# Kernel optimization log

Measured on AMD Instinct MI355X. Metric: run time of the kernel, lower is better.

The kernel has to match this reference:

```python
import jax, jax.numpy as jnp
import numpy as np

EPS = 1e-5

def _bn(x, g, b):
    # BatchNorm1d in training mode: biased batch variance, eps=1e-5
    mu = jnp.mean(x, axis=0)
    var = jnp.var(x, axis=0)
    return g * (x - mu) * jax.lax.rsqrt(var + EPS) + b

def _prelu(x, a):
    return jnp.where(x >= 0, x, a * x)

def setup_inputs() -> dict:
    key = jax.random.key(0)
    ks = jax.random.split(key, 32)
    B, MF, E = 4096, 128, 64
    f32 = jnp.float32

    def lin_w(k, o, i):
        bound = 1.0 / np.sqrt(i)
        return jax.random.uniform(k, (o, i), f32, -bound, bound)

    def lin_b(k, o, i):
        bound = 1.0 / np.sqrt(i)
        return jax.random.uniform(k, (o,), f32, -bound, bound)

    def exp_w(k, e, o, i):
        bound = 1.0 / np.sqrt(i)
        return jax.random.uniform(k, (e, o, i), f32, -bound, bound)

    def exp_b(k, e, o, i):
        bound = 1.0 / np.sqrt(i)
        return jax.random.uniform(k, (e, o), f32, -bound, bound)

    quarter = jnp.full((1,), 0.25, f32)  # PReLU default init
    return {
        'm0': jax.random.normal(ks[0], (B, MF), f32),
        'x0': jax.random.normal(ks[1], (B, 64), f32),
        'mW1': lin_w(ks[2], 256, 128), 'mb1': lin_b(ks[3], 256, 128),
        'mg1': jnp.ones((256,), f32), 'mbe1': jnp.zeros((256,), f32), 'ma1': quarter,
        'mW2': lin_w(ks[4], 128, 256), 'mb2': lin_b(ks[5], 128, 256),
        'mg2': jnp.ones((128,), f32), 'mbe2': jnp.zeros((128,), f32), 'ma2': quarter,
        'mW3': lin_w(ks[6], 64, 128), 'mb3': lin_b(ks[7], 64, 128),
        'mg3': jnp.ones((64,), f32), 'mbe3': jnp.zeros((64,), f32), 'ma3': quarter,
        'Wenc0': exp_w(ks[8], E, 256, 64), 'benc0': exp_b(ks[9], E, 256, 64),
        'Wenc1': exp_w(ks[10], E, 256, 256), 'benc1': exp_b(ks[11], E, 256, 256),
        'Wdec0': exp_w(ks[12], E, 256, 256), 'bdec0': exp_b(ks[13], E, 256, 256),
        'Wdec1': exp_w(ks[14], E, 64, 256), 'bdec1': exp_b(ks[15], E, 64, 256),
        'bng': jnp.ones((256,), f32), 'bnb': jnp.zeros((256,), f32), 'a': quarter,
    }

def reference(m0, x0, mW1, mb1, mg1, mbe1, ma1, mW2, mb2, mg2, mbe2, ma2,
              mW3, mb3, mg3, mbe3, ma3, Wenc0, benc0, Wenc1, benc1,
              Wdec0, bdec0, Wdec1, bdec1, bng, bnb, a):
    # m_encoder (MNet): Linear+BN+PReLU x3 -> per-sample expert weights [B, 64]
    h = _prelu(_bn(m0 @ mW1.T + mb1, mg1, mbe1), ma1)
    h = _prelu(_bn(h @ mW2.T + mb2, mg2, mbe2), ma2)
    w = _prelu(_bn(h @ mW3.T + mb3, mg3, mbe3), ma3)  # [B, E]

    w_sum = jnp.sum(w)           # scalar sum over all B*E, as in torch code
    wn = w / w_sum               # [B, E]

    def experts(z, W, b):
        # all-experts dense combine: sum_e wn[b,e] * (z @ W_e^T + b_e)
        h = jnp.einsum('bi,eoi->beo', z, W) + b  # [B, E, O]
        return jnp.einsum('beo,be->bo', h, wn)

    # encoder: depth=2, BN+PReLU after each layer (shared bn(256) and PReLU)
    z = _prelu(_bn(experts(x0, Wenc0, benc0), bng, bnb), a)
    z = _prelu(_bn(experts(z, Wenc1, benc1), bng, bnb), a)
    # decoder: BN+PReLU on all but last layer
    y = _prelu(_bn(experts(z, Wdec0, bdec0), bng, bnb), a)
    y = experts(y, Wdec1, bdec1)  # [B, 64]
    return y
```

## Files before the change

### kernel.cpp

```cpp
#include <hip/hip_runtime.h>
#include <stdint.h>

#define BATCH 4096
#define NEXP 64

typedef __bf16 bf16x8 __attribute__((ext_vector_type(8)));
typedef float f32x4 __attribute__((ext_vector_type(4)));
typedef float f32x8 __attribute__((ext_vector_type(8)));
typedef unsigned int u32x4 __attribute__((ext_vector_type(4)));
typedef unsigned short u16x4 __attribute__((ext_vector_type(4)));
typedef unsigned short u16x8 __attribute__((ext_vector_type(8)));

__device__ __forceinline__ unsigned short f2bf(float f) {
  unsigned u = __builtin_bit_cast(unsigned, f);
  u += 0x7fffu + ((u >> 16) & 1u);
  return (unsigned short)(u >> 16);
}

__device__ __forceinline__ void async_copy16(const void* g, void* l) {
  __builtin_amdgcn_global_load_lds(
      (const __attribute__((address_space(1))) void*)(uintptr_t)g,
      (__attribute__((address_space(3))) void*)(uintptr_t)l, 16, 0, 0);
}

enum { AM_PLAIN = 0, AM_BN = 1 };

template <int BM_, int BN_, int WR, int WC, int AMODE>
__global__ __launch_bounds__(256, 4) void gemm_k(
    const float* __restrict__ Af32, const float* __restrict__ scv,
    const float* __restrict__ shv, const float* __restrict__ alphaPtr,
    const unsigned short* __restrict__ PB, int K, int nsubsTot,
    float* __restrict__ Cp, const float* __restrict__ biasv, int N,
    int ktilesTot) {
  constexpr int MS = BM_ / 16;
  constexpr int NS = BN_ / 16;
  constexpr int WTM = BM_ / WR, WTN = BN_ / WC;
  constexpr int TM = WTM / 16, TN = WTN / 16;
  constexpr int PCH = MS / 2;

  __shared__ __align__(16) unsigned short As[2 * MS * 512];
  __shared__ __align__(16) unsigned short Bs[2 * NS * 512];

  const int tid = threadIdx.x;
  const int lane = tid & 63;
  const int wid = tid >> 6;
  const int wrow = wid / WC, wcol = wid % WC;

  const int m0 = blockIdx.x * BM_;
  const int ntile = blockIdx.y;
  const int n0 = ntile * BN_;

  float alpha = 0.f;
  if constexpr (AMODE == AM_BN) alpha = alphaPtr[0];

  f32x4 acc[TM][TN] = {};

  for (int kt = 0; kt < ktilesTot; ++kt) {
    const int k0 = kt * 64;

    for (int f = wid; f < 2 * NS; f += 4) {
      const int fkt = f / NS, fns = f % NS;
      const long fragIdx = (long)(k0 / 32 + fkt) * nsubsTot + (ntile * NS + fns);
      async_copy16(PB + fragIdx * 512 + lane * 8, &Bs[f * 512 + lane * 8]);
    }

#pragma unroll
    for (int p = 0; p < PCH; ++p) {
      const int id = p * 256 + tid;
      const int fA = id >> 6;
      const int q = id & 63;
      const int ksh = fA / MS, msub = fA % MS;
      const int kq = q >> 4, mrow = q & 15;
      const int m = msub * 16 + mrow;
      const int kg = k0 + ksh * 32 + kq * 8;
      const long mg = m0 + m;
      f32x8 vf;
      if constexpr (AMODE == AM_PLAIN) {
        const f32x4* src = (const f32x4*)(Af32 + mg * K + kg);
        f32x4 a0 = src[0], a1 = src[1];
#pragma unroll
        for (int j = 0; j < 4; ++j) { vf[j] = a0[j]; vf[4 + j] = a1[j]; }
      } else {
        const f32x4* src = (const f32x4*)(Af32 + mg * K + kg);
        f32x4 a0 = src[0], a1 = src[1];
        f32x4 s0 = *(const f32x4*)(scv + kg), s1 = *(const f32x4*)(scv + kg + 4);
        f32x4 h0 = *(const f32x4*)(shv + kg), h1 = *(const f32x4*)(shv + kg + 4);
#pragma unroll
        for (int j = 0; j < 4; ++j) {
          float v = fmaf(a0[j], s0[j], h0[j]);
          vf[j] = v >= 0.f ? v : alpha * v;
          float v2 = fmaf(a1[j], s1[j], h1[j]);
          vf[4 + j] = v2 >= 0.f ? v2 : alpha * v2;
        }
      }
      bf16x8 ob = __builtin_convertvector(vf, bf16x8);
      *(u16x8*)&As[id * 8] = __builtin_bit_cast(u16x8, ob);
    }
    __syncthreads();

#pragma unroll
    for (int ks = 0; ks < 2; ++ks) {
      bf16x8 af[TM], bfr[TN];
#pragma unroll
      for (int i = 0; i < TM; ++i) {
        const int msub = wrow * TM + i;
        af[i] = __builtin_bit_cast(
            bf16x8, *(const u32x4*)&As[(ks * MS + msub) * 512 + lane * 8]);
      }
#pragma unroll
      for (int j = 0; j < TN; ++j) {
        const int nsub = wcol * TN + j;
        bfr[j] = __builtin_bit_cast(
            bf16x8, *(const u32x4*)&Bs[(ks * NS + nsub) * 512 + lane * 8]);
      }
#pragma unroll
      for (int i = 0; i < TM; ++i)
#pragma unroll
        for (int j = 0; j < TN; ++j)
          acc[i][j] = __builtin_amdgcn_mfma_f32_16x16x32_bf16(af[i], bfr[j],
                                                              acc[i][j], 0, 0, 0);
    }
    __syncthreads();
  }

  const int q = lane >> 4, nn = lane & 15;
#pragma unroll
  for (int i = 0; i < TM; ++i) {
    const int rowb = m0 + wrow * WTM + i * 16 + q * 4;
#pragma unroll
    for (int j = 0; j < TN; ++j) {
      const int col = n0 + wcol * WTN + j * 16 + nn;
      const float bv = biasv ? biasv[col] : 0.f;
#pragma unroll
      for (int r = 0; r < 4; ++r)
        Cp[(long)(rowb + r) * N + col] = acc[i][j][r] + bv;
    }
  }
}

template <int BN_, int KE_, int EPB, int NTILE>
__global__ __launch_bounds__(256, 2) void egemm_k(
    const unsigned short* __restrict__ zpk, const float* __restrict__ wnT,
    const float* __restrict__ bias, const unsigned short* __restrict__ PB,
    float* __restrict__ Cbase, long partStride, int N, int nsubsTot) {
  constexpr int KT2 = KE_ / 32;
  constexpr int NS = BN_ / 16;
  constexpr int TN = NS / 4;
  constexpr int TM = 4;
  constexpr int NC = NTILE * (NEXP / EPB);
  constexpr int T = EPB * KT2;
  constexpr int U = ((KT2 & 3) == 0) ? 1 : (4 / KT2);

  const int tid = threadIdx.x, lane = tid & 63, wid = tid >> 6;
  const int bx = blockIdx.x;
  const int combo = bx % NC;
  const int mb = bx / NC;
  const int ntile = combo % NTILE;
  const int slice = combo / NTILE;
  const int e0 = slice * EPB;
  const int n0 = ntile * BN_;
  float* __restrict__ Cp = Cbase + (long)slice * partStride;
  const int nn = lane & 15, q = lane >> 4;

  float bvAll[EPB * TN];
#pragma unroll
  for (int ei = 0; ei < EPB; ++ei)
#pragma unroll
    for (int j = 0; j < TN; ++j)
      bvAll[ei * TN + j] =
          bias[(long)(e0 + ei) * N + n0 + wid * (TN * 16) + j * 16 + nn];

  const unsigned short* Aw = zpk + (long)mb * (KT2 * 4 * 512);
  u32x4 areg[TM][KT2];
#pragma unroll
  for (int i = 0; i < TM; ++i)
#pragma unroll
    for (int kt = 0; kt < KT2; ++kt)
      areg[i][kt] = *(const u32x4*)(Aw + (kt * 4 + i) * 512 + lane * 8);

  const long kstr = (long)nsubsTot * 512;
  const unsigned short* Bt = PB + (long)e0 * KT2 * kstr +
                             ((long)ntile * NS + wid * TN) * 512 + lane * 8;

  u32x4 ring[4][TN];
#pragma unroll
  for (int t = 0; t < 4; ++t)
#pragma unroll
    for (int j = 0; j < TN; ++j)
      ring[t][j] = *(const u32x4*)(Bt + (long)t * kstr + j * 512);

  f32x4 mainAcc[TM][TN] = {};

  for (int eb = 0; eb < EPB; eb += U) {
#pragma unroll
    for (int u = 0; u < U; ++u) {
      const int ei = eb + u;
      const int e = e0 + ei;
      f32x4 tmp[TM][TN];
#pragma unroll
      for (int j = 0; j < TN; ++j) {
        const float bv = bvAll[ei * TN + j];
        f32x4 t4 = {bv, bv, bv, bv};
#pragma unroll
        for (int i = 0; i < TM; ++i) tmp[i][j] = t4;
      }
#pragma unroll
      for (int kt = 0; kt < KT2; ++kt) {
        const int slot = (u * KT2 + kt) & 3;
#pragma unroll
        for (int i = 0; i < TM; ++i) {
          bf16x8 af = __builtin_bit_cast(bf16x8, areg[i][kt]);
#pragma unroll
          for (int j = 0; j < TN; ++j)
            tmp[i][j] = __builtin_amdgcn_mfma_f32_16x16x32_bf16(
                af, __builtin_bit_cast(bf16x8, ring[slot][j]), tmp[i][j], 0, 0,
                0);
        }
        {
          const int t = ei * KT2 + kt;
          const int tl = (t + 4 < T) ? (t + 4) : (T - 1);
#pragma unroll
          for (int j = 0; j < TN; ++j)
            ring[slot][j] = *(const u32x4*)(Bt + (long)tl * kstr + j * 512);
        }
      }
#pragma unroll
      for (int i = 0; i < TM; ++i) {
        const int rowb = mb * 64 + i * 16 + q * 4;
        f32x4 wn4 = *(const f32x4*)(wnT + (long)e * BATCH + rowb);
#pragma unroll
        for (int j = 0; j < TN; ++j) mainAcc[i][j] += wn4 * tmp[i][j];
      }
    }
  }

#pragma unroll
  for (int i = 0; i < TM; ++i) {
    const int rowb = mb * 64 + i * 16 + q * 4;
#pragma unroll
    for (int j = 0; j < TN; ++j) {
      const int col = n0 + wid * (TN * 16) + j * 16 + nn;
#pragma unroll
      for (int r = 0; r < 4; ++r)
        Cp[(long)(rowb + r) * N + col] = mainAcc[i][j][r];
    }
  }
}

__global__ void hstats_k(float* __restrict__ P, long partStride, int nparts,
                         int C, float* __restrict__ S1, float* __restrict__ S2) {
  const int c0 = blockIdx.x * 4;
  const int r0 = blockIdx.y * (BATCH / 8);
  f32x4 s = {0.f, 0.f, 0.f, 0.f}, s2 = {0.f, 0.f, 0.f, 0.f};
  for (int r = r0 + threadIdx.x; r < r0 + BATCH / 8; r += 256) {
    f32x4 x = *(const f32x4*)(P + (long)r * C + c0);
    for (int p = 1; p < nparts; ++p)
      x += *(const f32x4*)(P + p * partStride + (long)r * C + c0);
    *(f32x4*)(P + (long)r * C + c0) = x;
    s += x;
    s2 += x * x;
  }
  __shared__ f32x4 sb[256], qb[256];
  sb[threadIdx.x] = s;
  qb[threadIdx.x] = s2;
  __syncthreads();
  for (int st = 128; st > 0; st >>= 1) {
    if (threadIdx.x < st) {
      sb[threadIdx.x] += sb[threadIdx.x + st];
      qb[threadIdx.x] += qb[threadIdx.x + st];
    }
    __syncthreads();
  }
  if (threadIdx.x < 4) {
    atomicAdd(&S1[c0 + threadIdx.x], sb[0][threadIdx.x]);
    atomicAdd(&S2[c0 + threadIdx.x], qb[0][threadIdx.x]);
  }
}

__global__ void stats_k(const float* __restrict__ H, int C,
                        const float* __restrict__ g, const float* __restrict__ b,
                        float* __restrict__ scv, float* __restrict__ shv) {
  const int c0 = blockIdx.x * 4;
  f32x4 s = {0.f, 0.f, 0.f, 0.f}, s2 = {0.f, 0.f, 0.f, 0.f};
  for (int r = threadIdx.x; r < BATCH; r += 256) {
    f32x4 x = *(const f32x4*)(H + (long)r * C + c0);
    s += x;
    s2 += x * x;
  }
  __shared__ f32x4 sb[256], qb[256];
  sb[threadIdx.x] = s;
  qb[threadIdx.x] = s2;
  __syncthreads();
  for (int st = 128; st > 0; st >>= 1) {
    if (threadIdx.x < st) {
      sb[threadIdx.x] += sb[threadIdx.x + st];
      qb[threadIdx.x] += qb[threadIdx.x + st];
    }
    __syncthreads();
  }
  if (threadIdx.x < 4) {
    const int c = c0 + threadIdx.x;
    float mu = sb[0][threadIdx.x] * (1.f / BATCH);
    float var = qb[0][threadIdx.x] * (1.f / BATCH) - mu * mu;
    float isig = 1.f / sqrtf(var + 1e-5f);
    float sc_ = g[c] * isig;
    scv[c] = sc_;
    shv[c] = b[c] - mu * sc_;
  }
}

__global__ void zbuild_pk(const float* __restrict__ H,
                          const float* __restrict__ S1,
                          const float* __restrict__ S2,
                          const float* __restrict__ g,
                          const float* __restrict__ b,
                          const float* __restrict__ alphaPtr,
                          unsigned short* __restrict__ zpk) {
  const int c = blockIdx.x * 256 + threadIdx.x;
  const float alpha = alphaPtr[0];
  const int mb = c >> 11, r = c & 2047;
  const int kt = r >> 8, q2 = r & 255;
  const int msub = q2 >> 6, ln = q2 & 63;
  const int row = mb * 64 + msub * 16 + (ln & 15);
  const int col = kt * 32 + (ln >> 4) * 8;
  const float* src = H + (long)row * 256 + col;
  u16x8 o;
#pragma unroll
  for (int h = 0; h < 2; ++h) {
    f32x4 a = *(const f32x4*)(src + h * 4);
    f32x4 s1 = *(const f32x4*)(S1 + col + h * 4);
    f32x4 s2 = *(const f32x4*)(S2 + col + h * 4);
    f32x4 gv = *(const f32x4*)(g + col + h * 4);
    f32x4 bv = *(const f32x4*)(b + col + h * 4);
#pragma unroll
    for (int j = 0; j < 4; ++j) {
      float mu = s1[j] * (1.f / BATCH);
      float var = s2[j] * (1.f / BATCH) - mu * mu;
      float sc_ = gv[j] / sqrtf(var + 1e-5f);
      float sh_ = bv[j] - mu * sc_;
      float v = fmaf(a[j], sc_, sh_);
      v = v >= 0.f ? v : alpha * v;
      o[h * 4 + j] = f2bf(v);
    }
  }
  *(u16x8*)(zpk + (long)c * 8) = o;
}

__global__ void wbuild_k(const float* __restrict__ G, const float* __restrict__ scv,
                         const float* __restrict__ shv,
                         const float* __restrict__ alphaPtr,
                         float* __restrict__ w, float* __restrict__ wsum) {
  const int idx = blockIdx.x * 256 + threadIdx.x;
  const float alpha = alphaPtr[0];
  const int c0 = (idx * 4) & 63;
  f32x4 x = *(const f32x4*)(G + (long)idx * 4);
  f32x4 sv = *(const f32x4*)(scv + c0);
  f32x4 hv = *(const f32x4*)(shv + c0);
  f32x4 o;
  float part = 0.f;
#pragma unroll
  for (int j = 0; j < 4; ++j) {
    float v = fmaf(x[j], sv[j], hv[j]);
    v = v >= 0.f ? v : alpha * v;
    o[j] = v;
    part += v;
  }
  *(f32x4*)(w + (long)idx * 4) = o;
  __shared__ float sb[256];
  sb[threadIdx.x] = part;
  __syncthreads();
  for (int st = 128; st > 0; st >>= 1) {
    if (threadIdx.x < st) sb[threadIdx.x] += sb[threadIdx.x + st];
    __syncthreads();
  }
  if (threadIdx.x == 0) atomicAdd(wsum, sb[0]);
}

__global__ void wnTcast_k(const float* __restrict__ w,
                          const float* __restrict__ wsum,
                          float* __restrict__ wnT, const float* __restrict__ x0,
                          unsigned short* __restrict__ x0pk) {
  const int bx = blockIdx.x;
  if (bx < 1024) {
    const int idx = bx * 256 + threadIdx.x;
    const int e = idx >> 12, b = idx & 4095;
    wnT[idx] = w[(long)b * NEXP + e] * (1.0f / wsum[0]);
  } else {
    const int c = (bx - 1024) * 256 + threadIdx.x;
    const int mb = c >> 9, r = c & 511;
    const int kt = r >> 8, q2 = r & 255;
    const int msub = q2 >> 6, ln = q2 & 63;
    const int row = mb * 64 + msub * 16 + (ln & 15);
    const int col = kt * 32 + (ln >> 4) * 8;
    const float* src = x0 + (long)row * 64 + col;
    f32x4 a0 = *(const f32x4*)src, a1 = *(const f32x4*)(src + 4);
    u16x8 o;
#pragma unroll
    for (int j = 0; j < 4; ++j) {
      o[j] = f2bf(a0[j]);
      o[4 + j] = f2bf(a1[j]);
    }
    *(u16x8*)(x0pk + (long)c * 8) = o;
  }
}

__global__ void prepackall_k(
    const float* __restrict__ w0, const float* __restrict__ w1,
    const float* __restrict__ w2, const float* __restrict__ w3,
    const float* __restrict__ w4, const float* __restrict__ w5,
    const float* __restrict__ w6, unsigned short* __restrict__ PB) {
  const int t = blockIdx.x * 256 + threadIdx.x;
  const float* W;
  int nsubs, shI;
  long loc;
  if (t < 4096) { W = w0; nsubs = 16; shI = 7; loc = t; }
  else if (t < 8192) { W = w1; nsubs = 8; shI = 8; loc = t - 4096; }
  else if (t < 9216) { W = w2; nsubs = 4; shI = 7; loc = t - 8192; }
  else if (t < 140288) { W = w3; nsubs = 16; shI = 6; loc = t - 9216; }
  else if (t < 664576) { W = w4; nsubs = 16; shI = 8; loc = t - 140288; }
  else if (t < 1188864) { W = w5; nsubs = 16; shI = 8; loc = t - 664576; }
  else if (t < 1319936) { W = w6; nsubs = 4; shI = 8; loc = t - 1188864; }
  else return;
  const int lane = (int)(loc & 63);
  const long frag = loc >> 6;
  const int nsub = (int)(frag % nsubs);
  const long ktile = frag / nsubs;
  const int n = nsub * 16 + (lane & 15);
  const int k = (int)(ktile * 32 + (lane >> 4) * 8);
  const int e = k >> shI;
  const int i0 = k & ((1 << shI) - 1);
  const int O = nsubs * 16;
  const float* src = W + ((long)e * O + n) * (1 << shI) + i0;
  f32x4 a0 = *(const f32x4*)src, a1 = *(const f32x4*)(src + 4);
  u16x8 o;
#pragma unroll
  for (int j = 0; j < 4; ++j) {
    o[j] = f2bf(a0[j]);
    o[4 + j] = f2bf(a1[j]);
  }
  *(u16x8*)(PB + (long)t * 8) = o;
}

__global__ void reduceN_k(const float* __restrict__ P, long partStride, int nparts,
                          float* __restrict__ out, int total4) {
  const int idx = blockIdx.x * 256 + threadIdx.x;
  if (idx >= total4) return;
  f32x4 s = {0.f, 0.f, 0.f, 0.f};
  for (int p = 0; p < nparts; ++p)
    s += *(const f32x4*)(P + p * partStride + (long)idx * 4);
  *(f32x4*)(out + (long)idx * 4) = s;
}

extern "C" void kernel_launch(void* const* d_in, const int* in_sizes, int n_in,
                              void* d_out, int out_size, void* d_ws, size_t ws_size,
                              hipStream_t stream) {
  const float* m0 = (const float*)d_in[0];
  const float* x0 = (const float*)d_in[1];
  const float* mW1 = (const float*)d_in[2];
  const float* mb1 = (const float*)d_in[3];
  const float* mg1 = (const float*)d_in[4];
  const float* mbe1 = (const float*)d_in[5];
  const float* ma1 = (const float*)d_in[6];
  const float* mW2 = (const float*)d_in[7];
  const float* mb2 = (const float*)d_in[8];
  const float* mg2 = (const float*)d_in[9];
  const float* mbe2 = (const float*)d_in[10];
  const float* ma2 = (const float*)d_in[11];
  const float* mW3 = (const float*)d_in[12];
  const float* mb3 = (const float*)d_in[13];
  const float* mg3 = (const float*)d_in[14];
  const float* mbe3 = (const float*)d_in[15];
  const float* ma3 = (const float*)d_in[16];
  const float* Wenc0 = (const float*)d_in[17];
  const float* benc0 = (const float*)d_in[18];
  const float* Wenc1 = (const float*)d_in[19];
  const float* benc1 = (const float*)d_in[20];
  const float* Wdec0 = (const float*)d_in[21];
  const float* bdec0 = (const float*)d_in[22];
  const float* Wdec1 = (const float*)d_in[23];
  const float* bdec1 = (const float*)d_in[24];
  const float* bng = (const float*)d_in[25];
  const float* bnb = (const float*)d_in[26];
  const float* aexp = (const float*)d_in[27];

  const int SPL = 4;
  const int SPLD = 8;

  char* base = (char*)d_ws;
  size_t off = 0;
  auto alloc = [&](size_t bytes) {
    void* p = base + off;
    off = (off + bytes + 255) & ~(size_t)255;
    return p;
  };
  unsigned short* PB = (unsigned short*)alloc(1319936L * 16);
  const long CO_mW2 = 4096, CO_mW3 = 8192, CO_e0 = 9216, CO_e1 = 140288,
             CO_d0 = 664576, CO_d1 = 1188864;
  float* Pb = (float*)alloc((size_t)SPL * BATCH * 256 * 4);
  float* P0 = Pb;
  float* P1 = Pb + (long)BATCH * 256;
  unsigned short* zApk = (unsigned short*)alloc(BATCH * 256 * 2);
  unsigned short* zBpk = (unsigned short*)alloc(BATCH * 256 * 2);
  unsigned short* x0pk = (unsigned short*)alloc(BATCH * 64 * 2);
  float* wbuf = (float*)alloc(BATCH * 64 * 4);
  float* wnT = (float*)alloc((size_t)NEXP * BATCH * 4);
  float* scv = (float*)alloc(256 * 4);
  float* shv = (float*)alloc(256 * 4);
  float* zeroBuf = (float*)alloc(8192);
  float* wsum = zeroBuf;
  float* S1a = zeroBuf + 256, *S2a = zeroBuf + 512;
  float* S1b = zeroBuf + 768, *S2b = zeroBuf + 1024;
  float* S1c = zeroBuf + 1280, *S2c = zeroBuf + 1536;

  const dim3 blk(256);
  const long PS = BATCH * 256;

  hipMemsetAsync(zeroBuf, 0, 8192, stream);
  prepackall_k<<<5156, blk, 0, stream>>>(mW1, mW2, mW3, Wenc0, Wenc1, Wdec0,
                                         Wdec1, PB);

  gemm_k<64, 128, 2, 2, AM_PLAIN><<<dim3(64, 2, 1), blk, 0, stream>>>(
      m0, nullptr, nullptr, nullptr, PB, 128, 16, P0, mb1, 256, 2);
  stats_k<<<64, blk, 0, stream>>>(P0, 256, mg1, mbe1, scv, shv);
  gemm_k<64, 128, 2, 2, AM_BN><<<dim3(64, 1, 1), blk, 0, stream>>>(
      P0, scv, shv, ma1, PB + CO_mW2 * 8, 256, 8, P1, mb2, 128, 4);
  stats_k<<<32, blk, 0, stream>>>(P1, 128, mg2, mbe2, scv, shv);
  gemm_k<64, 64, 2, 2, AM_BN><<<dim3(64, 1, 1), blk, 0, stream>>>(
      P1, scv, shv, ma2, PB + CO_mW3 * 8, 128, 4, P0, mb3, 64, 2);
  stats_k<<<16, blk, 0, stream>>>(P0, 64, mg3, mbe3, scv, shv);
  wbuild_k<<<256, blk, 0, stream>>>(P0, scv, shv, ma3, wbuf, wsum);
  wnTcast_k<<<1152, blk, 0, stream>>>(wbuf, wsum, wnT, x0, x0pk);

  egemm_k<128, 64, 16, 2><<<dim3(512), blk, 0, stream>>>(
      x0pk, wnT, benc0, PB + CO_e0 * 8, Pb, PS, 256, 16);
  hstats_k<<<dim3(64, 8), blk, 0, stream>>>(Pb, PS, SPL, 256, S1a, S2a);
  zbuild_pk<<<512, blk, 0, stream>>>(Pb, S1a, S2a, bng, bnb, aexp, zApk);

  egemm_k<128, 256, 16, 2><<<dim3(512), blk, 0, stream>>>(
      zApk, wnT, benc1, PB + CO_e1 * 8, Pb, PS, 256, 16);
  hstats_k<<<dim3(64, 8), blk, 0, stream>>>(Pb, PS, SPL, 256, S1b, S2b);
  zbuild_pk<<<512, blk, 0, stream>>>(Pb, S1b, S2b, bng, bnb, aexp, zBpk);

  egemm_k<128, 256, 16, 2><<<dim3(512), blk, 0, stream>>>(
      zBpk, wnT, bdec0, PB + CO_d0 * 8, Pb, PS, 256, 16);
  hstats_k<<<dim3(64, 8), blk, 0, stream>>>(Pb, PS, SPL, 256, S1c, S2c);
  zbuild_pk<<<512, blk, 0, stream>>>(Pb, S1c, S2c, bng, bnb, aexp, zApk);

  egemm_k<64, 256, 8, 1><<<dim3(512), blk, 0, stream>>>(
      zApk, wnT, bdec1, PB + CO_d1 * 8, Pb, (long)BATCH * 64, 64, 4);
  reduceN_k<<<256, blk, 0, stream>>>(Pb, (long)BATCH * 64, SPLD, (float*)d_out,
                                     65536);

  (void)in_sizes; (void)n_in; (void)out_size; (void)ws_size;
}
```

Measured before the change: 410.8 us.

## Split expert GEMMs along K into halves and restructure partial-sum stats reduction

Adds a KHALVES template parameter to the expert GEMM so each block handles half of the K dimension, writing to separate partial buffers. This doubles the grid size, and halves the register-held A fragments, to improve occupancy and parallelism. It also rewrites hstats_k to use row-group blocks with full-width column coverage and fewer reduction barriers, and chooses the partition count from the workspace size. The cost is more partial-sum traffic, since the reduction kernels must read 8 or 16 partial buffers instead of 4 or 8.

```diff
diff --git a/kernel.cpp b/kernel.cpp
--- a/kernel.cpp
+++ b/kernel.cpp
@@ -138,16 +138,19 @@
   }
 }
 
-template <int BN_, int KE_, int EPB, int NTILE>
+template <int BN_, int KE_, int EPB, int NTILE, int KHALVES>
 __global__ __launch_bounds__(256, 2) void egemm_k(
     const unsigned short* __restrict__ zpk, const float* __restrict__ wnT,
     const float* __restrict__ bias, const unsigned short* __restrict__ PB,
     float* __restrict__ Cbase, long partStride, int N, int nsubsTot) {
-  constexpr int KT2 = KE_ / 32;
+  constexpr int KT2F = KE_ / 32;
+  constexpr int KT2 = KT2F / KHALVES;
+  constexpr int LK = (KT2 == 8) ? 3 : (KT2 == 4) ? 2 : 1;
   constexpr int NS = BN_ / 16;
   constexpr int TN = NS / 4;
   constexpr int TM = 4;
-  constexpr int NC = NTILE * (NEXP / EPB);
+  constexpr int S = NEXP / EPB;
+  constexpr int NC = NTILE * S * KHALVES;
   constexpr int T = EPB * KT2;
   constexpr int U = ((KT2 & 3) == 0) ? 1 : (4 / KT2);
 
@@ -156,57 +159,60 @@
   const int combo = bx % NC;
   const int mb = bx / NC;
   const int ntile = combo % NTILE;
-  const int slice = combo / NTILE;
+  const int rest = combo / NTILE;
+  const int slice = rest % S;
+  const int khalf = rest / S;
   const int e0 = slice * EPB;
   const int n0 = ntile * BN_;
-  float* __restrict__ Cp = Cbase + (long)slice * partStride;
+  float* __restrict__ Cp = Cbase + (long)(khalf * S + slice) * partStride;
   const int nn = lane & 15, q = lane >> 4;
-
-  float bvAll[EPB * TN];
-#pragma unroll
-  for (int ei = 0; ei < EPB; ++ei)
-#pragma unroll
-    for (int j = 0; j < TN; ++j)
-      bvAll[ei * TN + j] =
-          bias[(long)(e0 + ei) * N + n0 + wid * (TN * 16) + j * 16 + nn];
-
-  const unsigned short* Aw = zpk + (long)mb * (KT2 * 4 * 512);
+  const bool addBias = (KHALVES == 1) || (khalf == 0);
+
+  const unsigned short* zb =
+      zpk + (long)mb * (KT2F * 4 * 512) + (long)khalf * (KT2 * 4 * 512);
   u32x4 areg[TM][KT2];
 #pragma unroll
   for (int i = 0; i < TM; ++i)
 #pragma unroll
     for (int kt = 0; kt < KT2; ++kt)
-      areg[i][kt] = *(const u32x4*)(Aw + (kt * 4 + i) * 512 + lane * 8);
+      areg[i][kt] = *(const u32x4*)(zb + (kt * 4 + i) * 512 + lane * 8);
 
   const long kstr = (long)nsubsTot * 512;
-  const unsigned short* Bt = PB + (long)e0 * KT2 * kstr +
+  const unsigned short* Bq = PB + ((long)e0 * KT2F + khalf * KT2) * kstr +
                              ((long)ntile * NS + wid * TN) * 512 + lane * 8;
+  auto baddr = [&](int u) {
+    const int ei = u >> LK, kt = u & (KT2 - 1);
+    return Bq + ((long)ei * KT2F + kt) * kstr;
+  };
 
   u32x4 ring[4][TN];
 #pragma unroll
-  for (int t = 0; t < 4; ++t)
-#pragma unroll
-    for (int j = 0; j < TN; ++j)
-      ring[t][j] = *(const u32x4*)(Bt + (long)t * kstr + j * 512);
+  for (int t = 0; t < 4; ++t) {
+    const unsigned short* a = baddr(t < T ? t : T - 1);
+#pragma unroll
+    for (int j = 0; j < TN; ++j) ring[t][j] = *(const u32x4*)(a + j * 512);
+  }
 
   f32x4 mainAcc[TM][TN] = {};
 
   for (int eb = 0; eb < EPB; eb += U) {
 #pragma unroll
-    for (int u = 0; u < U; ++u) {
-      const int ei = eb + u;
+    for (int uu = 0; uu < U; ++uu) {
+      const int ei = eb + uu;
       const int e = e0 + ei;
       f32x4 tmp[TM][TN];
 #pragma unroll
       for (int j = 0; j < TN; ++j) {
-        const float bv = bvAll[ei * TN + j];
+        const float bv =
+            addBias ? bias[(long)e * N + n0 + wid * (TN * 16) + j * 16 + nn]
+                    : 0.f;
         f32x4 t4 = {bv, bv, bv, bv};
 #pragma unroll
         for (int i = 0; i < TM; ++i) tmp[i][j] = t4;
       }
 #pragma unroll
       for (int kt = 0; kt < KT2; ++kt) {
-        const int slot = (u * KT2 + kt) & 3;
+        const int slot = (uu * KT2 + kt) & 3;
 #pragma unroll
         for (int i = 0; i < TM; ++i) {
           bf16x8 af = __builtin_bit_cast(bf16x8, areg[i][kt]);
@@ -217,11 +223,12 @@
                 0);
         }
         {
-          const int t = ei * KT2 + kt;
-          const int tl = (t + 4 < T) ? (t + 4) : (T - 1);
+          const int u = ei * KT2 + kt;
+          const int un = (u + 4 < T) ? (u + 4) : (T - 1);
+          const unsigned short* a = baddr(un);
 #pragma unroll
           for (int j = 0; j < TN; ++j)
-            ring[slot][j] = *(const u32x4*)(Bt + (long)tl * kstr + j * 512);
+            ring[slot][j] = *(const u32x4*)(a + j * 512);
         }
       }
 #pragma unroll
@@ -248,15 +255,18 @@
 }
 
 __global__ void hstats_k(float* __restrict__ P, long partStride, int nparts,
-                         int C, float* __restrict__ S1, float* __restrict__ S2) {
-  const int c0 = blockIdx.x * 4;
-  const int r0 = blockIdx.y * (BATCH / 8);
+                         float* __restrict__ S1, float* __restrict__ S2) {
+  const int c0 = (threadIdx.x & 63) * 4;
+  const int rg = threadIdx.x >> 6;
+  const int rb = blockIdx.x * 8;
   f32x4 s = {0.f, 0.f, 0.f, 0.f}, s2 = {0.f, 0.f, 0.f, 0.f};
-  for (int r = r0 + threadIdx.x; r < r0 + BATCH / 8; r += 256) {
-    f32x4 x = *(const f32x4*)(P + (long)r * C + c0);
+#pragma unroll
+  for (int it = 0; it < 2; ++it) {
+    const long r = rb + it * 4 + rg;
+    f32x4 x = *(const f32x4*)(P + r * 256 + c0);
     for (int p = 1; p < nparts; ++p)
-      x += *(const f32x4*)(P + p * partStride + (long)r * C + c0);
-    *(f32x4*)(P + (long)r * C + c0) = x;
+      x += *(const f32x4*)(P + p * partStride + r * 256 + c0);
+    *(f32x4*)(P + r * 256 + c0) = x;
     s += x;
     s2 += x * x;
   }
@@ -264,16 +274,17 @@
   sb[threadIdx.x] = s;
   qb[threadIdx.x] = s2;
   __syncthreads();
-  for (int st = 128; st > 0; st >>= 1) {
-    if (threadIdx.x < st) {
-      sb[threadIdx.x] += sb[threadIdx.x + st];
-      qb[threadIdx.x] += qb[threadIdx.x + st];
-    }
-    __syncthreads();
-  }
-  if (threadIdx.x < 4) {
-    atomicAdd(&S1[c0 + threadIdx.x], sb[0][threadIdx.x]);
-    atomicAdd(&S2[c0 + threadIdx.x], qb[0][threadIdx.x]);
+  if (threadIdx.x < 64) {
+    f32x4 ts = sb[threadIdx.x] + sb[64 + threadIdx.x] + sb[128 + threadIdx.x] +
+               sb[192 + threadIdx.x];
+    f32x4 tq = qb[threadIdx.x] + qb[64 + threadIdx.x] + qb[128 + threadIdx.x] +
+               qb[192 + threadIdx.x];
+    const int c = threadIdx.x * 4;
+#pragma unroll
+    for (int j = 0; j < 4; ++j) {
+      atomicAdd(&S1[c + j], ts[j]);
+      atomicAdd(&S2[c + j], tq[j]);
+    }
   }
 }
 
@@ -483,8 +494,8 @@
   const float* bnb = (const float*)d_in[26];
   const float* aexp = (const float*)d_in[27];
 
-  const int SPL = 4;
-  const int SPLD = 8;
+  const bool big = ws_size >= (size_t)62 * 1024 * 1024;
+  const int NPARTS = big ? 8 : 4;
 
   char* base = (char*)d_ws;
   size_t off = 0;
@@ -496,7 +507,7 @@
   unsigned short* PB = (unsigned short*)alloc(1319936L * 16);
   const long CO_mW2 = 4096, CO_mW3 = 8192, CO_e0 = 9216, CO_e1 = 140288,
              CO_d0 = 664576, CO_d1 = 1188864;
-  float* Pb = (float*)alloc((size_t)SPL * BATCH * 256 * 4);
+  float* Pb = (float*)alloc((size_t)NPARTS * BATCH * 256 * 4);
   float* P0 = Pb;
   float* P1 = Pb + (long)BATCH * 256;
   unsigned short* zApk = (unsigned short*)alloc(BATCH * 256 * 2);
@@ -531,25 +542,47 @@
   wbuild_k<<<256, blk, 0, stream>>>(P0, scv, shv, ma3, wbuf, wsum);
   wnTcast_k<<<1152, blk, 0, stream>>>(wbuf, wsum, wnT, x0, x0pk);
 
-  egemm_k<128, 64, 16, 2><<<dim3(512), blk, 0, stream>>>(
-      x0pk, wnT, benc0, PB + CO_e0 * 8, Pb, PS, 256, 16);
-  hstats_k<<<dim3(64, 8), blk, 0, stream>>>(Pb, PS, SPL, 256, S1a, S2a);
-  zbuild_pk<<<512, blk, 0, stream>>>(Pb, S1a, S2a, bng, bnb, aexp, zApk);
-
-  egemm_k<128, 256, 16, 2><<<dim3(512), blk, 0, stream>>>(
-      zApk, wnT, benc1, PB + CO_e1 * 8, Pb, PS, 256, 16);
-  hstats_k<<<dim3(64, 8), blk, 0, stream>>>(Pb, PS, SPL, 256, S1b, S2b);
-  zbuild_pk<<<512, blk, 0, stream>>>(Pb, S1b, S2b, bng, bnb, aexp, zBpk);
-
-  egemm_k<128, 256, 16, 2><<<dim3(512), blk, 0, stream>>>(
-      zBpk, wnT, bdec0, PB + CO_d0 * 8, Pb, PS, 256, 16);
-  hstats_k<<<dim3(64, 8), blk, 0, stream>>>(Pb, PS, SPL, 256, S1c, S2c);
-  zbuild_pk<<<512, blk, 0, stream>>>(Pb, S1c, S2c, bng, bnb, aexp, zApk);
-
-  egemm_k<64, 256, 8, 1><<<dim3(512), blk, 0, stream>>>(
-      zApk, wnT, bdec1, PB + CO_d1 * 8, Pb, (long)BATCH * 64, 64, 4);
-  reduceN_k<<<256, blk, 0, stream>>>(Pb, (long)BATCH * 64, SPLD, (float*)d_out,
-                                     65536);
-
-  (void)in_sizes; (void)n_in; (void)out_size; (void)ws_size;
-}
+  if (big) {
+    egemm_k<128, 64, 16, 2, 1><<<dim3(512), blk, 0, stream>>>(
+        x0pk, wnT, benc0, PB + CO_e0 * 8, Pb, PS, 256, 16);
+    hstats_k<<<512, blk, 0, stream>>>(Pb, PS, 4, S1a, S2a);
+    zbuild_pk<<<512, blk, 0, stream>>>(Pb, S1a, S2a, bng, bnb, aexp, zApk);
+
+    egemm_k<128, 256, 16, 2, 2><<<dim3(1024), blk, 0, stream>>>(
+        zApk, wnT, benc1, PB + CO_e1 * 8, Pb, PS, 256, 16);
+    hstats_k<<<512, blk, 0, stream>>>(Pb, PS, 8, S1b, S2b);
+    zbuild_pk<<<512, blk, 0, stream>>>(Pb, S1b, S2b, bng, bnb, aexp, zBpk);
+
+    egemm_k<128, 256, 16, 2, 2><<<dim3(1024), blk, 0, stream>>>(
+        zBpk, wnT, bdec0, PB + CO_d0 * 8, Pb, PS, 256, 16);
+    hstats_k<<<512, blk, 0, stream>>>(Pb, PS, 8, S1c, S2c);
+    zbuild_pk<<<512, blk, 0, stream>>>(Pb, S1c, S2c, bng, bnb, aexp, zApk);
+
+    egemm_k<64, 256, 8, 1, 2><<<dim3(1024), blk, 0, stream>>>(
+        zApk, wnT, bdec1, PB + CO_d1 * 8, Pb, (long)BATCH * 64, 64, 4);
+    reduceN_k<<<256, blk, 0, stream>>>(Pb, (long)BATCH * 64, 16,
+                                       (float*)d_out, 65536);
+  } else {
+    egemm_k<128, 64, 32, 2, 1><<<dim3(256), blk, 0, stream>>>(
+        x0pk, wnT, benc0, PB + CO_e0 * 8, Pb, PS, 256, 16);
+    hstats_k<<<512, blk, 0, stream>>>(Pb, PS, 2, S1a, S2a);
+    zbuild_pk<<<512, blk, 0, stream>>>(Pb, S1a, S2a, bng, bnb, aexp, zApk);
+
+    egemm_k<128, 256, 32, 2, 2><<<dim3(512), blk, 0, stream>>>(
+        zApk, wnT, benc1, PB + CO_e1 * 8, Pb, PS, 256, 16);
+    hstats_k<<<512, blk, 0, stream>>>(Pb, PS, 4, S1b, S2b);
+    zbuild_pk<<<512, blk, 0, stream>>>(Pb, S1b, S2b, bng, bnb, aexp, zBpk);
+
+    egemm_k<128, 256, 32, 2, 2><<<dim3(512), blk, 0, stream>>>(
+        zBpk, wnT, bdec0, PB + CO_d0 * 8, Pb, PS, 256, 16);
+    hstats_k<<<512, blk, 0, stream>>>(Pb, PS, 4, S1c, S2c);
+    zbuild_pk<<<512, blk, 0, stream>>>(Pb, S1c, S2c, bng, bnb, aexp, zApk);
+
+    egemm_k<64, 256, 8, 1, 2><<<dim3(1024), blk, 0, stream>>>(
+        zApk, wnT, bdec1, PB + CO_d1 * 8, Pb, (long)BATCH * 64, 64, 4);
+    reduceN_k<<<256, blk, 0, stream>>>(Pb, (long)BATCH * 64, 16,
+                                       (float*)d_out, 65536);
+  }
+
+  (void)in_sizes; (void)n_in; (void)out_size;
+}
```

After: 522.5 us. 1.27x slower.
